# Kernel tuning notes

Measured on AMD Instinct MI355X. Metric: run time of the kernel, lower is better.

Reference implementation:

```python
import jax, jax.numpy as jnp
import numpy as np

N = 20000          # nodes
DEG = 8            # deterministic in-degree per node
E = N * DEG        # edges
IN_DIM = 16
HID = 128
EDGE_DIM = 8
OUT_DIM = 4
LN_EPS = 1e-5
# degree histogram has all mass at DEG -> avg log-degree = log(DEG + 1)
AVG_DEG_LOG = float(np.log(DEG + 1.0))


def _init(key, fan_in, fan_out):
    s = float(np.sqrt(2.0 / (fan_in + fan_out)))  # glorot-ish
    return jax.random.normal(key, (fan_in, fan_out), jnp.float32) * s


def setup_inputs() -> dict:
    key = jax.random.key(0)
    ks = jax.random.split(key, 24)
    x = jax.random.normal(ks[0], (N, IN_DIM), jnp.float32)
    src = jax.random.randint(ks[1], (E,), 0, N, jnp.int32)
    dst = (jnp.arange(E, dtype=jnp.int32) % N)  # every node has exactly DEG in-edges
    edge_index = jnp.stack([src, dst], axis=0)
    edge_attr = jax.random.normal(ks[2], (E, EDGE_DIM), jnp.float32)
    d = {"x": x, "edge_attr": edge_attr, "edge_index": edge_index}
    i = 3
    for l, fi in enumerate([IN_DIM, HID]):  # 2 PNAConv layers (num_layers=3)
        d[f"ew{l}"] = _init(ks[i], EDGE_DIM, fi); i += 1   # edge_encoder
        d[f"eb{l}"] = jnp.zeros((fi,), jnp.float32)
        d[f"pw{l}"] = _init(ks[i], 3 * fi, fi); i += 1     # pre_nn: cat(x_i,x_j,e)
        d[f"pb{l}"] = jnp.zeros((fi,), jnp.float32)
        d[f"qw{l}"] = _init(ks[i], 13 * fi, HID); i += 1   # post_nn: (4 aggr * 3 scalers + 1)*F_in
        d[f"qb{l}"] = jnp.zeros((HID,), jnp.float32)
        d[f"lw{l}"] = _init(ks[i], HID, HID); i += 1       # PNAConv.lin
        d[f"lb{l}"] = jnp.zeros((HID,), jnp.float32)
        d[f"g{l}"] = jnp.ones((HID,), jnp.float32)         # LayerNorm gamma
        d[f"b{l}"] = jnp.zeros((HID,), jnp.float32)        # LayerNorm beta
    d["hw"] = _init(ks[i], HID, OUT_DIM)
    d["hb"] = jnp.zeros((OUT_DIM,), jnp.float32)
    return d


def _pna_conv(x, src, dst, edge_attr, ew, eb, pw, pb, qw, qb, lw, lb):
    # messages: cat(x_i, x_j, edge_encoder(edge_attr)) -> pre MLP
    e = edge_attr @ ew + eb                                   # [E, F_in]
    h = jnp.concatenate([x[dst], x[src], e], axis=-1)         # [E, 3*F_in]
    h = h @ pw + pb                                           # [E, F_in]
    # multi-aggregator reduce by destination node
    deg = jax.ops.segment_sum(jnp.ones((E,), h.dtype), dst, num_segments=N)
    degc = jnp.maximum(deg, 1.0)[:, None]
    mean = jax.ops.segment_sum(h, dst, num_segments=N) / degc
    mean2 = jax.ops.segment_sum(h * h, dst, num_segments=N) / degc
    mx = jax.ops.segment_max(h, dst, num_segments=N)
    mn = jax.ops.segment_min(h, dst, num_segments=N)
    std = jnp.sqrt(jax.nn.relu(mean2 - mean * mean) + 1e-5)
    agg = jnp.concatenate([mean, mx, mn, std], axis=-1)       # [N, 4*F_in]
    # degree scalers: identity, amplification, attenuation (scaler-major layout)
    logd = jnp.log(deg + 1.0)[:, None]
    scaled = jnp.concatenate(
        [agg, agg * (logd / AVG_DEG_LOG), agg * (AVG_DEG_LOG / logd)], axis=-1
    )                                                         # [N, 12*F_in]
    out = jnp.concatenate([x, scaled], axis=-1) @ qw + qb     # post_nn, [N, F_out]
    return out @ lw + lb                                      # PNAConv.lin


def _ln(x, g, b):
    m = jnp.mean(x, axis=-1, keepdims=True)
    v = jnp.mean((x - m) ** 2, axis=-1, keepdims=True)
    return (x - m) / jnp.sqrt(v + LN_EPS) * g + b


def reference(x, edge_attr, ew0, eb0, pw0, pb0, qw0, qb0, lw0, lb0, g0, b0,
              ew1, eb1, pw1, pb1, qw1, qb1, lw1, lb1, g1, b1, hw, hb, edge_index):
    src, dst = edge_index[0], edge_index[1]
    h = _pna_conv(x, src, dst, edge_attr, ew0, eb0, pw0, pb0, qw0, qb0, lw0, lb0)
    h = jax.nn.relu(_ln(h, g0, b0))  # dropout is identity at inference
    h = _pna_conv(h, src, dst, edge_attr, ew1, eb1, pw1, pb1, qw1, qb1, lw1, lb1)
    h = jax.nn.relu(_ln(h, g1, b1))
    return h @ hw + hb               # head, [N, OUT_DIM]
```

## Files before the change

### kernel.cpp

```cpp
#include <hip/hip_runtime.h>
#include <math.h>

#define N_NODES 20000
#define N_EDGES 160000

typedef unsigned short ushort_t;
typedef __attribute__((ext_vector_type(8))) short short8v;
typedef __attribute__((ext_vector_type(4))) float f32x4;
typedef __attribute__((ext_vector_type(8))) float f32x8;

#define WS_We0  0
#define WS_b0m  128
#define WS_W0   256
#define WS_b0   10496
#define WS_We1  10624
#define WS_b1m  11648
#define WS_b1   11776
#define WS_WP1  11904
#define WS_WPTU 52864
#define WS_t0   69248
#define WS_u0   389248
#define WS_h0b  709248
#define WS_t1   1989248
#define WS_u1   4549248
#define WS_A0   7109248
#define WS_A1   7109248

__device__ inline ushort_t f2bf(float f) {
    union { float f; unsigned u; } v; v.f = f;
    unsigned r = v.u + 0x7FFFu + ((v.u >> 16) & 1u);
    return (ushort_t)(r >> 16);
}
__device__ inline float bf2f(short s) {
    union { unsigned u; float f; } v; v.u = ((unsigned)(ushort_t)s) << 16; return v.f;
}

__device__ __attribute__((noinline)) void prep_item(
    int tid, const float* __restrict__ x,
    const float* __restrict__ ew0, const float* __restrict__ eb0,
    const float* __restrict__ pw0, const float* __restrict__ pb0,
    const float* __restrict__ qw0, const float* __restrict__ qb0,
    const float* __restrict__ lw0, const float* __restrict__ lb0,
    const float* __restrict__ ew1, const float* __restrict__ eb1,
    const float* __restrict__ pw1, const float* __restrict__ pb1,
    const float* __restrict__ qw1, const float* __restrict__ qb1,
    const float* __restrict__ lw1, const float* __restrict__ lb1,
    float* __restrict__ ws)
{
    if (tid < 81920) {
        int r = tid >> 7, o = tid & 127;
        float acc = 0.f;
        for (int h = 0; h < 128; ++h) {
            float qr;
            if (r < 128) qr = qw1[r*128 + h];
            else {
                int s = r - 128;
                qr = qw1[(128+s)*128+h] + qw1[(640+s)*128+h] + qw1[(1152+s)*128+h];
            }
            acc += qr * lw1[h*128 + o];
        }
        int ct = o >> 4, ks = r >> 5;
        int l = (o & 15) | (((r >> 3) & 3) << 4);
        ((ushort_t*)(ws + WS_WP1))[(size_t)(((ct*20 + ks)*64) + l)*8 + (r & 7)] = f2bf(acc);
    } else if (tid < 82048) {
        int o = tid - 81920;
        float acc = lb1[o];
        for (int h = 0; h < 128; ++h) acc += qb1[h] * lw1[h*128 + o];
        ws[WS_b1 + o] = acc;
    } else if (tid < 92288) {
        int idx = tid - 82048; int r = idx >> 7, o = idx & 127;
        float acc = 0.f;
        for (int h = 0; h < 128; ++h) {
            float qr;
            if (r < 16) qr = qw0[r*128 + h];
            else {
                int s = r - 16;
                qr = qw0[(16+s)*128+h] + qw0[(80+s)*128+h] + qw0[(144+s)*128+h];
            }
            acc += qr * lw0[h*128 + o];
        }
        ws[WS_W0 + idx] = acc;
    } else if (tid < 92416) {
        int o = tid - 92288;
        float acc = lb0[o];
        for (int h = 0; h < 128; ++h) acc += qb0[h] * lw0[h*128 + o];
        ws[WS_b0 + o] = acc;
    } else if (tid < 93440) {
        int idx = tid - 92416; int c = idx >> 7, f = idx & 127;
        float acc = 0.f;
        for (int k = 0; k < 128; ++k) acc += ew1[c*128 + k] * pw1[(256+k)*128 + f];
        ws[WS_We1 + idx] = acc;
    } else if (tid < 93568) {
        int f = tid - 93440;
        float acc = pb1[f];
        for (int k = 0; k < 128; ++k) acc += eb1[k] * pw1[(256+k)*128 + f];
        ws[WS_b1m + f] = acc;
    } else if (tid < 93696) {
        int idx = tid - 93568; int c = idx >> 4, f = idx & 15;
        float acc = 0.f;
        for (int k = 0; k < 16; ++k) acc += ew0[c*16 + k] * pw0[(32+k)*16 + f];
        ws[WS_We0 + idx] = acc;
    } else if (tid < 93712) {
        int f = tid - 93696;
        float acc = pb0[f];
        for (int k = 0; k < 16; ++k) acc += eb0[k] * pw0[(32+k)*16 + f];
        ws[WS_b0m + f] = acc;
    } else if (tid < 126480) {
        int idx = tid - 93712;
        int r = idx >> 7, o = idx & 127;
        int part = r >> 7, rk = r & 127;
        int ct = part*8 + (o >> 4);
        int l = (o & 15) | (((rk >> 3) & 3) << 4);
        ((ushort_t*)(ws + WS_WPTU))[(size_t)(((ct*4 + (rk >> 5))*64) + l)*8 + (rk & 7)]
            = f2bf(pw1[r*128 + o]);
    } else if (tid < 446480) {
        int idx = tid - 126480; int i = idx >> 4, f = idx & 15;
        float acc = 0.f;
        for (int k = 0; k < 16; ++k) acc += x[i*16 + k] * pw0[k*16 + f];
        ws[WS_t0 + idx] = acc;
    } else if (tid < 766480) {
        int idx = tid - 446480; int i = idx >> 4, f = idx & 15;
        float acc = 0.f;
        for (int k = 0; k < 16; ++k) acc += x[i*16 + k] * pw0[(16+k)*16 + f];
        ws[WS_u0 + idx] = acc;
    }
}

__device__ __attribute__((noinline)) void agg0_tile(
    int tile, int t, const float* __restrict__ x, const float* __restrict__ ea,
    const int* __restrict__ src, float* __restrict__ ws)
{
    static __shared__ float ea_s0[16*8*8];
    static __shared__ int   src_s0[16*8];
    static __shared__ float We0_s0[128];
    static __shared__ float b0m_s0[16];
    const int i0 = tile * 16;
    __syncthreads();

    for (int idx = t; idx < 1024; idx += 256) {
        int k = idx >> 7; int rem = idx & 127; int n = rem >> 3, c = rem & 7;
        ea_s0[(n*8 + k)*8 + c] = ea[(i0 + n + k*N_NODES)*8 + c];
    }
    if (t < 128) {
        int k = t >> 4, n = t & 15;
        src_s0[n*8 + k] = src[i0 + n + k*N_NODES];
        We0_s0[t] = ws[WS_We0 + t];
    }
    if (t < 16) b0m_s0[t] = ws[WS_b0m + t];
    __syncthreads();

    const int n = t >> 4, f = t & 15;
    const int i = i0 + n;
    float base = ws[WS_t0 + i*16 + f] + b0m_s0[f];
    float s = 0.f, q = 0.f, mx = -1e30f, mn = 1e30f;
    for (int k = 0; k < 8; ++k) {
        int sj = src_s0[n*8 + k];
        float m = base + ws[WS_u0 + sj*16 + f];
        #pragma unroll
        for (int c = 0; c < 8; ++c) m += ea_s0[(n*8+k)*8 + c] * We0_s0[c*16 + f];
        s += m; q += m*m; mx = fmaxf(mx, m); mn = fminf(mn, m);
    }
    float mean = s * 0.125f, mean2 = q * 0.125f;
    float sd = sqrtf(fmaxf(mean2 - mean*mean, 0.f) + 1e-5f);
    float* A0 = ws + WS_A0 + (size_t)i * 80;
    A0[f]      = x[i*16 + f];
    A0[16 + f] = mean;
    A0[32 + f] = mx;
    A0[48 + f] = mn;
    A0[64 + f] = sd;
}

__device__ __attribute__((noinline)) void gemm0_tile(
    int tile, int t, const float* __restrict__ g0, const float* __restrict__ bln0,
    float* __restrict__ ws)
{
    static __shared__ float As[32][81];
    const int r0 = tile * 32;
    __syncthreads();
    const float* A = ws + WS_A0 + (size_t)r0 * 80;
    for (int idx = t; idx < 32*80; idx += 256) {
        int r = idx / 80, k = idx - r*80;
        As[r][k] = A[idx];
    }
    __syncthreads();
    const int tc = t & 31, tr = t >> 5;
    const int c0 = tc * 4;
    float acc[4][4] = {};
    const float* W = ws + WS_W0;
    #pragma unroll 4
    for (int k = 0; k < 80; ++k) {
        float4 b = *(const float4*)(W + k*128 + c0);
        #pragma unroll
        for (int rr = 0; rr < 4; ++rr) {
            float a = As[tr*4 + rr][k];
            acc[rr][0] += a*b.x; acc[rr][1] += a*b.y;
            acc[rr][2] += a*b.z; acc[rr][3] += a*b.w;
        }
    }
    float4 bias = *(const float4*)(ws + WS_b0 + c0);
    float4 g  = *(const float4*)(g0 + c0);
    float4 bb = *(const float4*)(bln0 + c0);
    ushort_t* h0b = (ushort_t*)(ws + WS_h0b);
    #pragma unroll
    for (int rr = 0; rr < 4; ++rr) {
        float v0 = acc[rr][0] + bias.x, v1 = acc[rr][1] + bias.y;
        float v2 = acc[rr][2] + bias.z, v3 = acc[rr][3] + bias.w;
        float sum = v0+v1+v2+v3;
        float sq  = v0*v0+v1*v1+v2*v2+v3*v3;
        #pragma unroll
        for (int off = 1; off < 32; off <<= 1) {
            sum += __shfl_xor(sum, off, 64);
            sq  += __shfl_xor(sq,  off, 64);
        }
        float mean = sum * (1.f/128.f);
        float var  = sq  * (1.f/128.f) - mean*mean;
        float rstd = rsqrtf(var + 1e-5f);
        ushort4 ob;
        ob.x = f2bf(fmaxf((v0-mean)*rstd*g.x + bb.x, 0.f));
        ob.y = f2bf(fmaxf((v1-mean)*rstd*g.y + bb.y, 0.f));
        ob.z = f2bf(fmaxf((v2-mean)*rstd*g.z + bb.z, 0.f));
        ob.w = f2bf(fmaxf((v3-mean)*rstd*g.w + bb.w, 0.f));
        *(ushort4*)(h0b + (size_t)(r0 + tr*4 + rr)*128 + c0) = ob;
    }
}

__device__ __attribute__((noinline)) void tu1_half(
    int tile, int part, int lane, float* __restrict__ ws)
{
    const int rowbase = tile * 16;
    const ushort_t* h0b = (const ushort_t*)(ws + WS_h0b);
    const ushort_t* WP  = (const ushort_t*)(ws + WS_WPTU);
    const int lr = lane & 15, lk = lane >> 4;
    const size_t arow = rowbase + lr;
    f32x4 acc[8];
    #pragma unroll
    for (int c = 0; c < 8; ++c) acc[c] = (f32x4){0.f,0.f,0.f,0.f};

    #pragma unroll
    for (int ks = 0; ks < 4; ++ks) {
        short8v a = *(const short8v*)(h0b + arow*128 + ks*32 + lk*8);
        #pragma unroll
        for (int c = 0; c < 8; ++c) {
            short8v b = *(const short8v*)(WP + ((size_t)((part*8 + c)*4 + ks)*64 + lane)*8);
            acc[c] = __builtin_amdgcn_mfma_f32_16x16x32_bf16(a, b, acc[c], 0, 0, 0);
        }
    }
    if (part == 0) {
        float* t1 = ws + WS_t1;
        #pragma unroll
        for (int c = 0; c < 8; ++c) {
            int cb = c*16 + lr;
            #pragma unroll
            for (int r = 0; r < 4; ++r) {
                int row = rowbase + lk*4 + r;
                t1[(size_t)row*128 + cb] = acc[c][r];
            }
        }
    } else {
        ushort_t* u1b = (ushort_t*)(ws + WS_u1);
        #pragma unroll
        for (int c = 0; c < 8; ++c) {
            int cb = c*16 + lr;
            #pragma unroll
            for (int r = 0; r < 4; ++r) {
                int row = rowbase + lk*4 + r;
                u1b[(size_t)row*128 + cb] = f2bf(acc[c][r]);
            }
        }
    }
}

__device__ __attribute__((noinline)) void agg1_tile(
    int tile, int t, const float* __restrict__ ea, const int* __restrict__ src,
    float* __restrict__ ws)
{
    static __shared__ float ea_s1[16*8*8];
    static __shared__ int   src_s1[128];
    static __shared__ float We1_s1[1024];
    static __shared__ float b1m_s1[128];
    const int i0 = tile * 16;
    __syncthreads();

    for (int idx = t; idx < 1024; idx += 256) {
        int k = idx >> 7; int rem = idx & 127; int n = rem >> 3, c = rem & 7;
        ea_s1[(n*8 + k)*8 + c] = ea[(i0 + n + k*N_NODES)*8 + c];
    }
    if (t < 128) {
        int k = t >> 4, n = t & 15;
        src_s1[n*8 + k] = src[i0 + n + k*N_NODES];
    }
    for (int idx = t; idx < 1024; idx += 256) We1_s1[idx] = ws[WS_We1 + idx];
    if (t < 128) b1m_s1[t] = ws[WS_b1m + t];
    __syncthreads();

    const int n = t >> 4, f0 = (t & 15) * 8;
    const int i = i0 + n;
    const ushort_t* u1b = (const ushort_t*)(ws + WS_u1);
    float base[8], sm[8], sq[8], mx[8], mn[8];
    #pragma unroll
    for (int e = 0; e < 8; ++e) {
        base[e] = ws[WS_t1 + (size_t)i*128 + f0 + e] + b1m_s1[f0 + e];
        sm[e] = 0.f; sq[e] = 0.f; mx[e] = -1e30f; mn[e] = 1e30f;
    }
    for (int k = 0; k < 8; ++k) {
        int sj = src_s1[n*8 + k];
        short8v uv = *(const short8v*)(u1b + (size_t)sj*128 + f0);
        float m[8];
        #pragma unroll
        for (int e = 0; e < 8; ++e) m[e] = base[e] + bf2f(uv[e]);
        #pragma unroll
        for (int c = 0; c < 8; ++c) {
            float a = ea_s1[(n*8 + k)*8 + c];
            #pragma unroll
            for (int e = 0; e < 8; ++e) m[e] += a * We1_s1[c*128 + f0 + e];
        }
        #pragma unroll
        for (int e = 0; e < 8; ++e) {
            sm[e] += m[e]; sq[e] += m[e]*m[e];
            mx[e] = fmaxf(mx[e], m[e]); mn[e] = fminf(mn[e], m[e]);
        }
    }
    ushort_t* A1 = (ushort_t*)(ws + WS_A1);
    short8v vm, vx, vn, vs;
    #pragma unroll
    for (int e = 0; e < 8; ++e) {
        float mean = sm[e]*0.125f, m2 = sq[e]*0.125f;
        float sd = sqrtf(fmaxf(m2 - mean*mean, 0.f) + 1e-5f);
        vm[e] = (short)f2bf(mean);
        vx[e] = (short)f2bf(mx[e]);
        vn[e] = (short)f2bf(mn[e]);
        vs[e] = (short)f2bf(sd);
    }
    size_t b = (size_t)i*512 + f0;
    *(short8v*)(A1 + b)       = vm;
    *(short8v*)(A1 + b + 128) = vx;
    *(short8v*)(A1 + b + 256) = vn;
    *(short8v*)(A1 + b + 384) = vs;
}

struct KArgs {
    const float *x, *ea; const int* src;
    const float *ew0,*eb0,*pw0,*pb0,*qw0,*qb0,*lw0,*lb0,*g0,*bl0;
    const float *ew1,*eb1,*pw1,*pb1,*qw1,*qb1,*lw1,*lb1,*g1,*bl1;
    const float *hw,*hb;
    float* ws; float* out;
};

__global__ __launch_bounds__(256) void k_prep(KArgs a) {
    int tid = blockIdx.x*256 + threadIdx.x;
    prep_item(tid, a.x, a.ew0, a.eb0, a.pw0, a.pb0, a.qw0, a.qb0, a.lw0, a.lb0,
              a.ew1, a.eb1, a.pw1, a.pb1, a.qw1, a.qb1, a.lw1, a.lb1, a.ws);
}

__global__ __launch_bounds__(256) void k_mid(KArgs a) {
    const int b = blockIdx.x, t = threadIdx.x;
    agg0_tile(b*2,     t, a.x, a.ea, a.src, a.ws);
    agg0_tile(b*2 + 1, t, a.x, a.ea, a.src, a.ws);
    gemm0_tile(b, t, a.g0, a.bl0, a.ws);
    __syncthreads();
    const int w = t >> 6;
    tu1_half(b*2 + (w >> 1), w & 1, t & 63, a.ws);
}

__global__ __launch_bounds__(256) void k_tail(KArgs a) {
    const int b = blockIdx.x, t = threadIdx.x;
    float* ws = a.ws;

    agg1_tile(b, t, a.ea, a.src, ws);
    __syncthreads();

    static __shared__ float redS[4][16], redQ[4][16];
    static __shared__ f32x4 redP[4][16];
    const int w = t >> 6, lane = t & 63;
    const int lr = lane & 15, lk = lane >> 4;
    const int rowbase = b * 16;
    const int row = rowbase + lr;
    const ushort_t* h0b = (const ushort_t*)(ws + WS_h0b);
    const ushort_t* A1  = (const ushort_t*)(ws + WS_A1);
    const ushort_t* WP  = (const ushort_t*)(ws + WS_WP1);

    f32x4 acc[2];
    acc[0] = (f32x4){0.f,0.f,0.f,0.f};
    acc[1] = (f32x4){0.f,0.f,0.f,0.f};

    #pragma unroll
    for (int kw = 0; kw < 4; ++kw) {
        short8v av = *(const short8v*)(h0b + (size_t)row*128 + kw*32 + lk*8);
        #pragma unroll
        for (int c = 0; c < 2; ++c) {
            int ct = w*2 + c;
            short8v bv = *(const short8v*)(WP + (size_t)((ct*20 + kw)*64 + lane)*8);
            acc[c] = __builtin_amdgcn_mfma_f32_16x16x32_bf16(av, bv, acc[c], 0, 0, 0);
        }
    }
    #pragma unroll 4
    for (int ks = 0; ks < 16; ++ks) {
        short8v av = *(const short8v*)(A1 + (size_t)row*512 + ks*32 + lk*8);
        #pragma unroll
        for (int c = 0; c < 2; ++c) {
            int ct = w*2 + c;
            short8v bv = *(const short8v*)(WP + (size_t)((ct*20 + 4 + ks)*64 + lane)*8);
            acc[c] = __builtin_amdgcn_mfma_f32_16x16x32_bf16(av, bv, acc[c], 0, 0, 0);
        }
    }

    float bc[2], gc[2], bbc[2]; f32x4 hwc[2];
    #pragma unroll
    for (int c = 0; c < 2; ++c) {
        int col = (w*2 + c)*16 + lr;
        bc[c]  = ws[WS_b1 + col];
        gc[c]  = a.g1[col];
        bbc[c] = a.bl1[col];
        hwc[c] = *(const f32x4*)(a.hw + col*4);
    }

    #pragma unroll
    for (int r = 0; r < 4; ++r) {
        float s = 0.f, q = 0.f;
        #pragma unroll
        for (int c = 0; c < 2; ++c) {
            float v = acc[c][r] + bc[c];
            s += v; q += v*v;
        }
        #pragma unroll
        for (int off = 1; off < 16; off <<= 1) {
            s += __shfl_xor(s, off, 64);
            q += __shfl_xor(q, off, 64);
        }
        if (lr == 0) { redS[w][lk*4 + r] = s; redQ[w][lk*4 + r] = q; }
    }
    __syncthreads();

    #pragma unroll
    for (int r = 0; r < 4; ++r) {
        int orow = lk*4 + r;
        float s_tot = redS[0][orow] + redS[1][orow] + redS[2][orow] + redS[3][orow];
        float q_tot = redQ[0][orow] + redQ[1][orow] + redQ[2][orow] + redQ[3][orow];
        float mean = s_tot * (1.f/128.f);
        float var  = q_tot * (1.f/128.f) - mean*mean;
        float rstd = rsqrtf(var + 1e-5f);
        f32x4 po = (f32x4){0.f,0.f,0.f,0.f};
        #pragma unroll
        for (int c = 0; c < 2; ++c) {
            float v = acc[c][r] + bc[c];
            float o = fmaxf((v-mean)*rstd*gc[c] + bbc[c], 0.f);
            po += o * hwc[c];
        }
        #pragma unroll
        for (int off = 1; off < 16; off <<= 1) {
            po.x += __shfl_xor(po.x, off, 64);
            po.y += __shfl_xor(po.y, off, 64);
            po.z += __shfl_xor(po.z, off, 64);
            po.w += __shfl_xor(po.w, off, 64);
        }
        if (lr == 0) redP[w][orow] = po;
    }
    __syncthreads();

    if (w == 0 && lr == 0) {
        f32x4 hb4 = *(const f32x4*)a.hb;
        #pragma unroll
        for (int r = 0; r < 4; ++r) {
            int orow = lk*4 + r;
            f32x4 res = redP[0][orow] + redP[1][orow] + redP[2][orow] + redP[3][orow] + hb4;
            *(f32x4*)(a.out + (size_t)(rowbase + orow)*4) = res;
        }
    }
}

extern "C" void kernel_launch(void* const* d_in, const int* in_sizes, int n_in,
                              void* d_out, int out_size, void* d_ws, size_t ws_size,
                              hipStream_t stream)
{
    KArgs a;
    a.x    = (const float*)d_in[0];
    a.ea   = (const float*)d_in[1];
    a.src  = (const int*)d_in[2];
    a.ew0  = (const float*)d_in[3];
    a.eb0  = (const float*)d_in[4];
    a.pw0  = (const float*)d_in[5];
    a.pb0  = (const float*)d_in[6];
    a.qw0  = (const float*)d_in[7];
    a.qb0  = (const float*)d_in[8];
    a.lw0  = (const float*)d_in[9];
    a.lb0  = (const float*)d_in[10];
    a.g0   = (const float*)d_in[11];
    a.bl0  = (const float*)d_in[12];
    a.ew1  = (const float*)d_in[13];
    a.eb1  = (const float*)d_in[14];
    a.pw1  = (const float*)d_in[15];
    a.pb1  = (const float*)d_in[16];
    a.qw1  = (const float*)d_in[17];
    a.qb1  = (const float*)d_in[18];
    a.lw1  = (const float*)d_in[19];
    a.lb1  = (const float*)d_in[20];
    a.g1   = (const float*)d_in[21];
    a.bl1  = (const float*)d_in[22];
    a.hw   = (const float*)d_in[23];
    a.hb   = (const float*)d_in[24];
    a.ws   = (float*)d_ws;
    a.out  = (float*)d_out;

    k_prep<<<2995, 256, 0, stream>>>(a);
    k_mid <<< 625, 256, 0, stream>>>(a);
    k_tail<<<1250, 256, 0, stream>>>(a);
}
```

Measured before the change: 108.5 us.

## Split tail kernel into 8-row, 128-thread blocks for more parallelism

The final fused kernel (layer-1 aggregation, post-MLP GEMM, LayerNorm and head) now processes 8 nodes per 128-thread block instead of 16 nodes per 256-thread block, launching twice as many blocks. Each of the two waves covers four 16-column MFMA tiles, and the 16-row MFMA input duplicates the 8 real rows so only the first 8 outputs are written. The aim is better occupancy and load balance across CUs. In exchange, half of the MFMA work is wasted and the packed weight operand is fetched twice as often per node.

```diff
diff --git a/kernel.cpp b/kernel.cpp
--- a/kernel.cpp
+++ b/kernel.cpp
@@ -270,27 +270,27 @@
     }
 }
 
-__device__ __attribute__((noinline)) void agg1_tile(
+__device__ __attribute__((noinline)) void agg1_tile128(
     int tile, int t, const float* __restrict__ ea, const int* __restrict__ src,
     float* __restrict__ ws)
 {
-    static __shared__ float ea_s1[16*8*8];
-    static __shared__ int   src_s1[128];
-    static __shared__ float We1_s1[1024];
-    static __shared__ float b1m_s1[128];
-    const int i0 = tile * 16;
-    __syncthreads();
-
-    for (int idx = t; idx < 1024; idx += 256) {
-        int k = idx >> 7; int rem = idx & 127; int n = rem >> 3, c = rem & 7;
-        ea_s1[(n*8 + k)*8 + c] = ea[(i0 + n + k*N_NODES)*8 + c];
-    }
-    if (t < 128) {
-        int k = t >> 4, n = t & 15;
-        src_s1[n*8 + k] = src[i0 + n + k*N_NODES];
-    }
-    for (int idx = t; idx < 1024; idx += 256) We1_s1[idx] = ws[WS_We1 + idx];
-    if (t < 128) b1m_s1[t] = ws[WS_b1m + t];
+    static __shared__ float ea_t[8*8*8];
+    static __shared__ int   src_t[64];
+    static __shared__ float We1_t[1024];
+    static __shared__ float b1m_t[128];
+    const int i0 = tile * 8;
+    __syncthreads();
+
+    for (int idx = t; idx < 512; idx += 128) {
+        int k = idx >> 6; int rem = idx & 63; int n = rem >> 3, c = rem & 7;
+        ea_t[(n*8 + k)*8 + c] = ea[(size_t)(i0 + n + k*N_NODES)*8 + c];
+    }
+    if (t < 64) {
+        int k = t >> 3, n = t & 7;
+        src_t[n*8 + k] = src[i0 + n + k*N_NODES];
+    }
+    for (int idx = t; idx < 1024; idx += 128) We1_t[idx] = ws[WS_We1 + idx];
+    if (t < 128) b1m_t[t] = ws[WS_b1m + t];
     __syncthreads();
 
     const int n = t >> 4, f0 = (t & 15) * 8;
@@ -299,20 +299,20 @@
     float base[8], sm[8], sq[8], mx[8], mn[8];
     #pragma unroll
     for (int e = 0; e < 8; ++e) {
-        base[e] = ws[WS_t1 + (size_t)i*128 + f0 + e] + b1m_s1[f0 + e];
+        base[e] = ws[WS_t1 + (size_t)i*128 + f0 + e] + b1m_t[f0 + e];
         sm[e] = 0.f; sq[e] = 0.f; mx[e] = -1e30f; mn[e] = 1e30f;
     }
     for (int k = 0; k < 8; ++k) {
-        int sj = src_s1[n*8 + k];
+        int sj = src_t[n*8 + k];
         short8v uv = *(const short8v*)(u1b + (size_t)sj*128 + f0);
         float m[8];
         #pragma unroll
         for (int e = 0; e < 8; ++e) m[e] = base[e] + bf2f(uv[e]);
         #pragma unroll
         for (int c = 0; c < 8; ++c) {
-            float a = ea_s1[(n*8 + k)*8 + c];
+            float a = ea_t[(n*8 + k)*8 + c];
             #pragma unroll
-            for (int e = 0; e < 8; ++e) m[e] += a * We1_s1[c*128 + f0 + e];
+            for (int e = 0; e < 8; ++e) m[e] += a * We1_t[c*128 + f0 + e];
         }
         #pragma unroll
         for (int e = 0; e < 8; ++e) {
@@ -362,33 +362,33 @@
     tu1_half(b*2 + (w >> 1), w & 1, t & 63, a.ws);
 }
 
-__global__ __launch_bounds__(256) void k_tail(KArgs a) {
+__global__ __launch_bounds__(128, 4) void k_tail(KArgs a) {
     const int b = blockIdx.x, t = threadIdx.x;
     float* ws = a.ws;
 
-    agg1_tile(b, t, a.ea, a.src, ws);
-    __syncthreads();
-
-    static __shared__ float redS[4][16], redQ[4][16];
-    static __shared__ f32x4 redP[4][16];
+    agg1_tile128(b, t, a.ea, a.src, ws);
+    __syncthreads();
+
+    static __shared__ float redS[2][16], redQ[2][16];
+    static __shared__ f32x4 redP[16];
     const int w = t >> 6, lane = t & 63;
     const int lr = lane & 15, lk = lane >> 4;
-    const int rowbase = b * 16;
-    const int row = rowbase + lr;
+    const int rowbase = b * 8;
+    const int row = rowbase + (lr & 7);
     const ushort_t* h0b = (const ushort_t*)(ws + WS_h0b);
     const ushort_t* A1  = (const ushort_t*)(ws + WS_A1);
     const ushort_t* WP  = (const ushort_t*)(ws + WS_WP1);
 
-    f32x4 acc[2];
-    acc[0] = (f32x4){0.f,0.f,0.f,0.f};
-    acc[1] = (f32x4){0.f,0.f,0.f,0.f};
+    f32x4 acc[4];
+    #pragma unroll
+    for (int c = 0; c < 4; ++c) acc[c] = (f32x4){0.f,0.f,0.f,0.f};
 
     #pragma unroll
     for (int kw = 0; kw < 4; ++kw) {
         short8v av = *(const short8v*)(h0b + (size_t)row*128 + kw*32 + lk*8);
         #pragma unroll
-        for (int c = 0; c < 2; ++c) {
-            int ct = w*2 + c;
+        for (int c = 0; c < 4; ++c) {
+            int ct = w*4 + c;
             short8v bv = *(const short8v*)(WP + (size_t)((ct*20 + kw)*64 + lane)*8);
             acc[c] = __builtin_amdgcn_mfma_f32_16x16x32_bf16(av, bv, acc[c], 0, 0, 0);
         }
@@ -397,17 +397,17 @@
     for (int ks = 0; ks < 16; ++ks) {
         short8v av = *(const short8v*)(A1 + (size_t)row*512 + ks*32 + lk*8);
         #pragma unroll
-        for (int c = 0; c < 2; ++c) {
-            int ct = w*2 + c;
+        for (int c = 0; c < 4; ++c) {
+            int ct = w*4 + c;
             short8v bv = *(const short8v*)(WP + (size_t)((ct*20 + 4 + ks)*64 + lane)*8);
             acc[c] = __builtin_amdgcn_mfma_f32_16x16x32_bf16(av, bv, acc[c], 0, 0, 0);
         }
     }
 
-    float bc[2], gc[2], bbc[2]; f32x4 hwc[2];
-    #pragma unroll
-    for (int c = 0; c < 2; ++c) {
-        int col = (w*2 + c)*16 + lr;
+    float bc[4], gc[4], bbc[4]; f32x4 hwc[4];
+    #pragma unroll
+    for (int c = 0; c < 4; ++c) {
+        int col = (w*4 + c)*16 + lr;
         bc[c]  = ws[WS_b1 + col];
         gc[c]  = a.g1[col];
         bbc[c] = a.bl1[col];
@@ -418,7 +418,7 @@
     for (int r = 0; r < 4; ++r) {
         float s = 0.f, q = 0.f;
         #pragma unroll
-        for (int c = 0; c < 2; ++c) {
+        for (int c = 0; c < 4; ++c) {
             float v = acc[c][r] + bc[c];
             s += v; q += v*v;
         }
@@ -431,17 +431,18 @@
     }
     __syncthreads();
 
+    f32x4 poarr[4];
     #pragma unroll
     for (int r = 0; r < 4; ++r) {
         int orow = lk*4 + r;
-        float s_tot = redS[0][orow] + redS[1][orow] + redS[2][orow] + redS[3][orow];
-        float q_tot = redQ[0][orow] + redQ[1][orow] + redQ[2][orow] + redQ[3][orow];
+        float s_tot = redS[0][orow] + redS[1][orow];
+        float q_tot = redQ[0][orow] + redQ[1][orow];
         float mean = s_tot * (1.f/128.f);
         float var  = q_tot * (1.f/128.f) - mean*mean;
         float rstd = rsqrtf(var + 1e-5f);
         f32x4 po = (f32x4){0.f,0.f,0.f,0.f};
         #pragma unroll
-        for (int c = 0; c < 2; ++c) {
+        for (int c = 0; c < 4; ++c) {
             float v = acc[c][r] + bc[c];
             float o = fmaxf((v-mean)*rstd*gc[c] + bbc[c], 0.f);
             po += o * hwc[c];
@@ -453,7 +454,8 @@
             po.z += __shfl_xor(po.z, off, 64);
             po.w += __shfl_xor(po.w, off, 64);
         }
-        if (lr == 0) redP[w][orow] = po;
+        poarr[r] = po;
+        if (w == 1 && lr == 0) redP[orow] = po;
     }
     __syncthreads();
 
@@ -462,8 +464,10 @@
         #pragma unroll
         for (int r = 0; r < 4; ++r) {
             int orow = lk*4 + r;
-            f32x4 res = redP[0][orow] + redP[1][orow] + redP[2][orow] + redP[3][orow] + hb4;
-            *(f32x4*)(a.out + (size_t)(rowbase + orow)*4) = res;
+            if (orow < 8) {
+                f32x4 res = poarr[r] + redP[orow] + hb4;
+                *(f32x4*)(a.out + (size_t)(rowbase + orow)*4) = res;
+            }
         }
     }
 }
@@ -503,5 +507,5 @@
 
     k_prep<<<2995, 256, 0, stream>>>(a);
     k_mid <<< 625, 256, 0, stream>>>(a);
-    k_tail<<<1250, 256, 0, stream>>>(a);
-}
+    k_tail<<<2500, 128, 0, stream>>>(a);
+}
```

After: 145.9 us. 34.5% more time.

## Split tail into separate aggregation and GEMM kernels with 32-row tiles and prefetch

Applied to the files above, without the earlier changes.

The fused tail kernel is split in two. One kernel runs the layer-1 aggregation; the other runs the post-NN GEMM with LayerNorm and the head. The GEMM kernel now takes 32 rows per block, with each wave covering 4 column tiles instead of 2, so each A fragment is reused across more MFMAs. A and B fragments for the next k-step are prefetched in registers to hide load latency. This costs an extra kernel launch and a round trip of the aggregation output through global memory, and uses more registers.

```diff
diff --git a/kernel.cpp b/kernel.cpp
--- a/kernel.cpp
+++ b/kernel.cpp
@@ -7,7 +7,6 @@
 typedef unsigned short ushort_t;
 typedef __attribute__((ext_vector_type(8))) short short8v;
 typedef __attribute__((ext_vector_type(4))) float f32x4;
-typedef __attribute__((ext_vector_type(8))) float f32x8;
 
 #define WS_We0  0
 #define WS_b0m  128
@@ -362,52 +361,57 @@
     tu1_half(b*2 + (w >> 1), w & 1, t & 63, a.ws);
 }
 
-__global__ __launch_bounds__(256) void k_tail(KArgs a) {
+__global__ __launch_bounds__(256) void k_agg1(KArgs a) {
+    agg1_tile(blockIdx.x, threadIdx.x, a.ea, a.src, a.ws);
+}
+
+__global__ __launch_bounds__(256) void k_gemm1(KArgs a) {
+    static __shared__ float redS[2][2][16], redQ[2][2][16];
+    static __shared__ f32x4 redP[2][16];
     const int b = blockIdx.x, t = threadIdx.x;
     float* ws = a.ws;
-
-    agg1_tile(b, t, a.ea, a.src, ws);
-    __syncthreads();
-
-    static __shared__ float redS[4][16], redQ[4][16];
-    static __shared__ f32x4 redP[4][16];
     const int w = t >> 6, lane = t & 63;
+    const int rt = w >> 1, chalf = w & 1;
     const int lr = lane & 15, lk = lane >> 4;
-    const int rowbase = b * 16;
-    const int row = rowbase + lr;
+    const int rowbase = b * 32;
+    const int row = rowbase + rt*16 + lr;
     const ushort_t* h0b = (const ushort_t*)(ws + WS_h0b);
     const ushort_t* A1  = (const ushort_t*)(ws + WS_A1);
     const ushort_t* WP  = (const ushort_t*)(ws + WS_WP1);
-
-    f32x4 acc[2];
-    acc[0] = (f32x4){0.f,0.f,0.f,0.f};
-    acc[1] = (f32x4){0.f,0.f,0.f,0.f};
-
-    #pragma unroll
-    for (int kw = 0; kw < 4; ++kw) {
-        short8v av = *(const short8v*)(h0b + (size_t)row*128 + kw*32 + lk*8);
-        #pragma unroll
-        for (int c = 0; c < 2; ++c) {
-            int ct = w*2 + c;
-            short8v bv = *(const short8v*)(WP + (size_t)((ct*20 + kw)*64 + lane)*8);
-            acc[c] = __builtin_amdgcn_mfma_f32_16x16x32_bf16(av, bv, acc[c], 0, 0, 0);
-        }
-    }
-    #pragma unroll 4
-    for (int ks = 0; ks < 16; ++ks) {
-        short8v av = *(const short8v*)(A1 + (size_t)row*512 + ks*32 + lk*8);
-        #pragma unroll
-        for (int c = 0; c < 2; ++c) {
-            int ct = w*2 + c;
-            short8v bv = *(const short8v*)(WP + (size_t)((ct*20 + 4 + ks)*64 + lane)*8);
-            acc[c] = __builtin_amdgcn_mfma_f32_16x16x32_bf16(av, bv, acc[c], 0, 0, 0);
-        }
-    }
-
-    float bc[2], gc[2], bbc[2]; f32x4 hwc[2];
-    #pragma unroll
-    for (int c = 0; c < 2; ++c) {
-        int col = (w*2 + c)*16 + lr;
+    const size_t aoff_h = (size_t)row*128 + lk*8;
+    const size_t aoff_a = (size_t)row*512 + lk*8;
+
+    f32x4 acc[4];
+    #pragma unroll
+    for (int c = 0; c < 4; ++c) acc[c] = (f32x4){0.f,0.f,0.f,0.f};
+
+    short8v aN = *(const short8v*)(h0b + aoff_h);
+    short8v bN0 = *(const short8v*)(WP + (size_t)(((chalf*4+0)*20)*64 + lane)*8);
+    short8v bN1 = *(const short8v*)(WP + (size_t)(((chalf*4+1)*20)*64 + lane)*8);
+    short8v bN2 = *(const short8v*)(WP + (size_t)(((chalf*4+2)*20)*64 + lane)*8);
+    short8v bN3 = *(const short8v*)(WP + (size_t)(((chalf*4+3)*20)*64 + lane)*8);
+    #pragma unroll
+    for (int ksu = 0; ksu < 20; ++ksu) {
+        short8v av = aN, bv0 = bN0, bv1 = bN1, bv2 = bN2, bv3 = bN3;
+        if (ksu < 19) {
+            const int kn = ksu + 1;
+            aN = (kn < 4) ? *(const short8v*)(h0b + aoff_h + kn*32)
+                          : *(const short8v*)(A1 + aoff_a + (kn-4)*32);
+            bN0 = *(const short8v*)(WP + (size_t)(((chalf*4+0)*20 + kn)*64 + lane)*8);
+            bN1 = *(const short8v*)(WP + (size_t)(((chalf*4+1)*20 + kn)*64 + lane)*8);
+            bN2 = *(const short8v*)(WP + (size_t)(((chalf*4+2)*20 + kn)*64 + lane)*8);
+            bN3 = *(const short8v*)(WP + (size_t)(((chalf*4+3)*20 + kn)*64 + lane)*8);
+        }
+        acc[0] = __builtin_amdgcn_mfma_f32_16x16x32_bf16(av, bv0, acc[0], 0, 0, 0);
+        acc[1] = __builtin_amdgcn_mfma_f32_16x16x32_bf16(av, bv1, acc[1], 0, 0, 0);
+        acc[2] = __builtin_amdgcn_mfma_f32_16x16x32_bf16(av, bv2, acc[2], 0, 0, 0);
+        acc[3] = __builtin_amdgcn_mfma_f32_16x16x32_bf16(av, bv3, acc[3], 0, 0, 0);
+    }
+
+    float bc[4], gc[4], bbc[4]; f32x4 hwc[4];
+    #pragma unroll
+    for (int c = 0; c < 4; ++c) {
+        int col = (chalf*4 + c)*16 + lr;
         bc[c]  = ws[WS_b1 + col];
         gc[c]  = a.g1[col];
         bbc[c] = a.bl1[col];
@@ -418,7 +422,7 @@
     for (int r = 0; r < 4; ++r) {
         float s = 0.f, q = 0.f;
         #pragma unroll
-        for (int c = 0; c < 2; ++c) {
+        for (int c = 0; c < 4; ++c) {
             float v = acc[c][r] + bc[c];
             s += v; q += v*v;
         }
@@ -427,21 +431,22 @@
             s += __shfl_xor(s, off, 64);
             q += __shfl_xor(q, off, 64);
         }
-        if (lr == 0) { redS[w][lk*4 + r] = s; redQ[w][lk*4 + r] = q; }
-    }
-    __syncthreads();
-
+        if (lr == 0) { redS[rt][chalf][lk*4 + r] = s; redQ[rt][chalf][lk*4 + r] = q; }
+    }
+    __syncthreads();
+
+    f32x4 poarr[4];
     #pragma unroll
     for (int r = 0; r < 4; ++r) {
         int orow = lk*4 + r;
-        float s_tot = redS[0][orow] + redS[1][orow] + redS[2][orow] + redS[3][orow];
-        float q_tot = redQ[0][orow] + redQ[1][orow] + redQ[2][orow] + redQ[3][orow];
+        float s_tot = redS[rt][0][orow] + redS[rt][1][orow];
+        float q_tot = redQ[rt][0][orow] + redQ[rt][1][orow];
         float mean = s_tot * (1.f/128.f);
         float var  = q_tot * (1.f/128.f) - mean*mean;
         float rstd = rsqrtf(var + 1e-5f);
         f32x4 po = (f32x4){0.f,0.f,0.f,0.f};
         #pragma unroll
-        for (int c = 0; c < 2; ++c) {
+        for (int c = 0; c < 4; ++c) {
             float v = acc[c][r] + bc[c];
             float o = fmaxf((v-mean)*rstd*gc[c] + bbc[c], 0.f);
             po += o * hwc[c];
@@ -453,17 +458,18 @@
             po.z += __shfl_xor(po.z, off, 64);
             po.w += __shfl_xor(po.w, off, 64);
         }
-        if (lr == 0) redP[w][orow] = po;
-    }
-    __syncthreads();
-
-    if (w == 0 && lr == 0) {
+        poarr[r] = po;
+        if (chalf == 1 && lr == 0) redP[rt][orow] = po;
+    }
+    __syncthreads();
+
+    if (chalf == 0 && lr == 0) {
         f32x4 hb4 = *(const f32x4*)a.hb;
         #pragma unroll
         for (int r = 0; r < 4; ++r) {
             int orow = lk*4 + r;
-            f32x4 res = redP[0][orow] + redP[1][orow] + redP[2][orow] + redP[3][orow] + hb4;
-            *(f32x4*)(a.out + (size_t)(rowbase + orow)*4) = res;
+            f32x4 res = poarr[r] + redP[rt][orow] + hb4;
+            *(f32x4*)(a.out + (size_t)(rowbase + rt*16 + orow)*4) = res;
         }
     }
 }
@@ -501,7 +507,8 @@
     a.ws   = (float*)d_ws;
     a.out  = (float*)d_out;
 
-    k_prep<<<2995, 256, 0, stream>>>(a);
-    k_mid <<< 625, 256, 0, stream>>>(a);
-    k_tail<<<1250, 256, 0, stream>>>(a);
-}
+    k_prep <<<2995, 256, 0, stream>>>(a);
+    k_mid  <<< 625, 256, 0, stream>>>(a);
+    k_agg1 <<<1250, 256, 0, stream>>>(a);
+    k_gemm1<<< 625, 256, 0, stream>>>(a);
+}
```

After: 99.46 us, median of 2. 8.3% less time.
